# Optimization experiments

Hardware: AMD Instinct MI355X
Metric: run time of the kernel (lower is better)

## Reference

```python
import jax, jax.numpy as jnp
import numpy as np
import math

C = 256
GROUPS = 8
EPS = 1e-5


def setup_inputs() -> dict:
    key = jax.random.key(0)
    ks = jax.random.split(key, 12)
    b, c, h, w = 4, C, 64, 64
    s = 1.0 / math.sqrt(c)
    return {
        "x": jax.random.normal(ks[0], (b, c, h, w), dtype=jnp.float32),
        "gamma": jax.random.normal(ks[1], (c,), dtype=jnp.float32) * 0.1 + 1.0,
        "beta": jax.random.normal(ks[2], (c,), dtype=jnp.float32) * 0.1,
        "wq": jax.random.normal(ks[3], (c, c), dtype=jnp.float32) * s,
        "bq": jnp.zeros((c,), dtype=jnp.float32),
        "wk": jax.random.normal(ks[4], (c, c), dtype=jnp.float32) * s,
        "bk": jnp.zeros((c,), dtype=jnp.float32),
        "wv": jax.random.normal(ks[5], (c, c), dtype=jnp.float32) * s,
        "bv": jnp.zeros((c,), dtype=jnp.float32),
        "wp": jax.random.normal(ks[6], (c, c), dtype=jnp.float32) * s,
        "bp": jnp.zeros((c,), dtype=jnp.float32),
    }


def _group_norm(x, gamma, beta):
    b, c, h, w = x.shape
    xg = x.reshape(b, GROUPS, c // GROUPS, h * w)
    mean = xg.mean(axis=(2, 3), keepdims=True)
    var = xg.var(axis=(2, 3), keepdims=True)
    xn = ((xg - mean) * jax.lax.rsqrt(var + EPS)).reshape(b, c, h, w)
    return xn * gamma[None, :, None, None] + beta[None, :, None, None]


def _conv1x1(x, w, b):
    # 1x1 conv == per-pixel channel GEMM
    return jnp.einsum('oc,bchw->bohw', w, x) + b[None, :, None, None]


def reference(x, gamma, beta, wq, bq, wk, bk, wv, bv, wp, bp):
    b, c, h, w = x.shape
    n = h * w
    xn = _group_norm(x, gamma, beta)
    q = _conv1x1(xn, wq, bq).reshape(b, c, n)  # [b,c,n]
    k = _conv1x1(xn, wk, bk).reshape(b, c, n)
    v = _conv1x1(xn, wv, bv).reshape(b, c, n)
    scale = 1.0 / math.sqrt(c)
    scores = jnp.einsum('bcn,bcm->bnm', q, k) * scale  # [b,n,n]
    attn = jax.nn.softmax(scores, axis=-1)
    out = jnp.einsum('bnm,bcm->bcn', attn, v).reshape(b, c, h, w)
    return _conv1x1(out, wp, bp) + x
```

## Files before the change

kernel.cpp:

```cpp
#include <hip/hip_runtime.h>
#include <hip/hip_bf16.h>
#include <math.h>


#define CCH 256
#define NPIX 4096
#define NB 4
#define NG 8
#define EPS 1e-5f
#define NCHUNK 4

typedef __attribute__((ext_vector_type(8))) short short8;
typedef __attribute__((ext_vector_type(4))) short short4v;
typedef __attribute__((ext_vector_type(4))) float f32x4;
typedef __attribute__((ext_vector_type(16))) float f32x16;
typedef unsigned short ushort_t;
typedef unsigned char u8;

#define GLD16(g, l) __builtin_amdgcn_global_load_lds( \
    (const __attribute__((address_space(1))) unsigned int*)(g), \
    (__attribute__((address_space(3))) unsigned int*)(l), 16, 0, 0)

__device__ inline ushort_t f2bf(float x) {
    union { float f; unsigned u; } c; c.f = x;
    unsigned r = c.u + 0x7FFFu + ((c.u >> 16) & 1u);
    return (ushort_t)(r >> 16);
}
__device__ inline float bf2f(ushort_t h) {
    union { unsigned u; float f; } c; c.u = ((unsigned)h) << 16;
    return c.f;
}
__device__ inline u8 f2fp8(float x) {
    return (u8)(__builtin_amdgcn_cvt_pk_fp8_f32(x, x, 0, false) & 0xff);
}
__device__ inline long mk64(unsigned lo, unsigned hi) {
    return (long)(((unsigned long long)hi << 32) | lo);
}

__global__ __launch_bounds__(256) void gn1w(const float* __restrict__ x,
                                            const float* __restrict__ wq,
                                            const float* __restrict__ wk,
                                            const float* __restrict__ wv,
                                            const float* __restrict__ wp,
                                            float* __restrict__ part,
                                            ushort_t* __restrict__ wbf,
                                            ushort_t* __restrict__ wpbf) {
    int bid = blockIdx.x;
    int t = threadIdx.x;
    if (bid >= 256) {
        int widx = bid - 256;
        int wi = widx >> 6;
        const float* src = wi == 0 ? wq : wi == 1 ? wk : wi == 2 ? wv : wp;
        ushort_t* dst = wi == 3 ? wpbf : wbf + wi * 65536;
        int i = (widx & 63) * 1024 + t * 4;
        float4 v = *(const float4*)(src + i);
        short4v o;
        o[0] = (short)f2bf(v.x); o[1] = (short)f2bf(v.y);
        o[2] = (short)f2bf(v.z); o[3] = (short)f2bf(v.w);
        *(short4v*)(dst + i) = o;
        return;
    }
    int bg = bid >> 3;
    int slice = bid & 7;
    const float* base = x + (size_t)bg * 32 * NPIX + (size_t)slice * 16384;
    float s = 0.f, sq = 0.f;
    for (int i = t; i < 4096; i += 256) {
        float4 v = ((const float4*)base)[i];
        s  += v.x + v.y + v.z + v.w;
        sq += v.x*v.x + v.y*v.y + v.z*v.z + v.w*v.w;
    }
    for (int off = 32; off; off >>= 1) {
        s  += __shfl_down(s,  off);
        sq += __shfl_down(sq, off);
    }
    __shared__ float red[8];
    int wid = t >> 6;
    if ((t & 63) == 0) { red[wid*2] = s; red[wid*2+1] = sq; }
    __syncthreads();
    if (t == 0) {
        float ts = 0.f, tq = 0.f;
        for (int wv2 = 0; wv2 < 4; wv2++) { ts += red[wv2*2]; tq += red[wv2*2+1]; }
        part[bid*2] = ts; part[bid*2+1] = tq;
    }
}

__global__ __launch_bounds__(256) void gn_transpose(const float* __restrict__ x,
                                                    const float* __restrict__ part,
                                                    const float* __restrict__ gamma,
                                                    const float* __restrict__ beta,
                                                    ushort_t* __restrict__ xnT) {
    __shared__ float T[64][69];
    __shared__ float gmean[2], grstd[2];
    int t = threadIdx.x;
    int nBase = blockIdx.x * 64;
    int cBase = blockIdx.y * 64;
    int b = blockIdx.z;
    if (t < 2) {
        int g = (cBase >> 5) + t;
        float s = 0.f, sq = 0.f;
        for (int i = 0; i < 8; i++) {
            s  += part[((b*NG + g)*8 + i)*2];
            sq += part[((b*NG + g)*8 + i)*2 + 1];
        }
        const float inv = 1.f / 131072.f;
        float mean = s * inv;
        float var = sq * inv - mean * mean;
        gmean[t] = mean;
        grstd[t] = rsqrtf(var + EPS);
    }
    __syncthreads();
    const float* xb = x + (size_t)b * CCH * NPIX;
    int n4  = (t & 15) * 4;
    int cc0 = (t >> 4) * 4;
    for (int i = 0; i < 4; i++) {
        int cc = cc0 + i;
        int c = cBase + cc;
        int gi = cc >> 5;
        float ga = gamma[c] * grstd[gi];
        float be = beta[c] - gmean[gi] * ga;
        float4 v = *(const float4*)&xb[(size_t)c * NPIX + nBase + n4];
        T[cc][n4+0] = v.x * ga + be;
        T[cc][n4+1] = v.y * ga + be;
        T[cc][n4+2] = v.z * ga + be;
        T[cc][n4+3] = v.w * ga + be;
    }
    __syncthreads();
    int nn  = t >> 2;
    int ci0 = (t & 3) * 16;
    short8 o0, o1;
    for (int j = 0; j < 8; j++) {
        o0[j] = (short)f2bf(T[ci0 + j][nn]);
        o1[j] = (short)f2bf(T[ci0 + 8 + j][nn]);
    }
    ushort_t* dst = xnT + ((size_t)b * NPIX + nBase + nn) * CCH + cBase + ci0;
    *(short8*)dst = o0;
    *((short8*)dst + 1) = o1;
}

__global__ __launch_bounds__(256, 2) void qkv3(const ushort_t* __restrict__ xnT,
                                               const ushort_t* __restrict__ wbf,
                                               const float* __restrict__ bq,
                                               const float* __restrict__ bk,
                                               const float* __restrict__ bv,
                                               u8* __restrict__ qT,
                                               u8* __restrict__ kT,
                                               u8* __restrict__ vv) {
    __shared__ __align__(16) ushort_t As[2][4096];
    __shared__ __align__(16) ushort_t Bs[2][4096];
    int t = threadIdx.x;
    int w = t >> 6, l = t & 63, quad = l >> 4, l16 = l & 15;
    int z = blockIdx.z;
    const ushort_t* A; const ushort_t* B; int mBase, nBase;
    if (z < 2) { A = xnT; B = wbf + z * 65536; mBase = blockIdx.x * 128; nBase = blockIdx.y * 128; }
    else       { A = wbf + 131072; B = xnT;    mBase = blockIdx.y * 128; nBase = blockIdx.x * 128; }
    int m0 = (w & 1) * 64, n0 = (w >> 1) * 64;

    const f32x4 fz = {0.f, 0.f, 0.f, 0.f};
    f32x4 acc[4][4];
    #pragma unroll
    for (int i = 0; i < 4; i++)
        #pragma unroll
        for (int j = 0; j < 4; j++) acc[i][j] = fz;

    int srow = t >> 2;
    int slc  = (t & 3) ^ ((t >> 2) & 3);
    int sldso = (t >> 6) * 512;

    #pragma unroll
    for (int j = 0; j < 2; j++) {
        int row = 64*j + srow;
        GLD16(A + (size_t)(mBase + row) * 256 + slc * 8, &As[0][j*2048 + sldso]);
        GLD16(B + (size_t)(nBase + row) * 256 + slc * 8, &Bs[0][j*2048 + sldso]);
    }
    int buf = 0;
    for (int kb = 0; kb < 8; kb++) {
        __syncthreads();
        if (kb < 7) {
            #pragma unroll
            for (int j = 0; j < 2; j++) {
                int row = 64*j + srow;
                GLD16(A + (size_t)(mBase + row) * 256 + (kb+1)*32 + slc * 8, &As[buf^1][j*2048 + sldso]);
                GLD16(B + (size_t)(nBase + row) * 256 + (kb+1)*32 + slc * 8, &Bs[buf^1][j*2048 + sldso]);
            }
        }
        short8 af[4], bfr[4];
        #pragma unroll
        for (int mb = 0; mb < 4; mb++)
            af[mb] = *(short8*)&As[buf][(m0 + mb*16 + l16)*32 + ((quad ^ (l16 & 3)) * 8)];
        #pragma unroll
        for (int nb = 0; nb < 4; nb++)
            bfr[nb] = *(short8*)&Bs[buf][(n0 + nb*16 + l16)*32 + ((quad ^ (l16 & 3)) * 8)];
        #pragma unroll
        for (int mb = 0; mb < 4; mb++)
            #pragma unroll
            for (int nb = 0; nb < 4; nb++)
                acc[mb][nb] = __builtin_amdgcn_mfma_f32_16x16x32_bf16(af[mb], bfr[nb], acc[mb][nb], 0, 0, 0);
        buf ^= 1;
    }
    if (z < 2) {
        const float* bias = z ? bk : bq;
        u8* C = z ? kT : qT;
        #pragma unroll
        for (int nb = 0; nb < 4; nb++) {
            int n = nBase + n0 + nb*16 + l16;
            float bb = bias[n];
            #pragma unroll
            for (int mb = 0; mb < 4; mb++)
                #pragma unroll
                for (int r = 0; r < 4; r++) {
                    int m = mBase + m0 + mb*16 + quad*4 + r;
                    C[(size_t)m * 256 + n] = f2fp8(acc[mb][nb][r] + bb);
                }
        }
    } else {
        #pragma unroll
        for (int mb = 0; mb < 4; mb++)
            #pragma unroll
            for (int r = 0; r < 4; r++) {
                int m = mBase + m0 + mb*16 + quad*4 + r;
                float bb = bv[m];
                #pragma unroll
                for (int nb = 0; nb < 4; nb++) {
                    int n = nBase + n0 + nb*16 + l16;
                    vv[((size_t)(n >> 12) * 256 + m) * 4096 + (n & 4095)] = f2fp8(acc[mb][nb][r] + bb);
                }
            }
    }
}

__global__ __launch_bounds__(128, 2) void flash_attn(const u8* __restrict__ qT,
                                                     const u8* __restrict__ kT,
                                                     const u8* __restrict__ vv,
                                                     ushort_t* __restrict__ Op0,
                                                     ushort_t* __restrict__ Op1,
                                                     ushort_t* __restrict__ Op2,
                                                     ushort_t* __restrict__ Op3,
                                                     float* __restrict__ lsum) {
    __shared__ __align__(16) u8 Ks[2][8192];
    __shared__ __align__(16) u8 Vs[2][8192];
    int t = threadIdx.x;
    int w = t >> 6, l = t & 63;
    int l32 = l & 31, hl = l >> 5;
    int qBase = blockIdx.x * 64, chunk = blockIdx.y, b = blockIdx.z;
    int qw = qBase + w * 32;

    long qf[16];
    {
        const u8* qrow = qT + ((size_t)b * NPIX + qw + l32) * 256 + hl * 8;
        #pragma unroll
        for (int cb = 0; cb < 16; cb++) qf[cb] = *(const long*)(qrow + cb * 16);
    }

    f32x16 accO[8];
    #pragma unroll
    for (int i = 0; i < 8; i++)
        #pragma unroll
        for (int r = 0; r < 16; r++) accO[i][r] = 0.f;
    float lqa = 0.f;

    const u8* kbase = kT + (size_t)b * NPIX * 256;
    const u8* vbase = vv + (size_t)b * 256 * NPIX;

    const float SC = 0.0625f * 1.44269504089f;
    int mStart = chunk * (NPIX / NCHUNK);
    int mEnd = mStart + NPIX / NCHUNK;

    int kkv[4], kcb[4], vc[4], vs[4];
    #pragma unroll
    for (int j = 0; j < 4; j++) {
        int n = j*128 + t;
        kkv[j] = n >> 4; kcb[j] = (n & 15) ^ (kkv[j] & 15);
        vc[j]  = n >> 1; vs[j]  = (n & 1) ^ ((vc[j] >> 2) & 1);
    }

    #pragma unroll
    for (int j = 0; j < 4; j++) {
        int n = j*128 + t;
        GLD16(kbase + (size_t)(mStart + kkv[j]) * 256 + kcb[j] * 16, &Ks[0][n*16]);
        GLD16(vbase + (size_t)vc[j] * NPIX + mStart + vs[j] * 16, &Vs[0][n*16]);
    }
    int buf = 0;
    for (int mBase = mStart; mBase < mEnd; mBase += 32) {
        __syncthreads();
        if (mBase + 32 < mEnd) {
            #pragma unroll
            for (int j = 0; j < 4; j++) {
                int n = j*128 + t;
                GLD16(kbase + (size_t)(mBase + 32 + kkv[j]) * 256 + kcb[j] * 16, &Ks[buf^1][n*16]);
                GLD16(vbase + (size_t)vc[j] * NPIX + mBase + 32 + vs[j] * 16, &Vs[buf^1][n*16]);
            }
        }
        f32x16 sTa, sTb;
        #pragma unroll
        for (int r = 0; r < 16; r++) { sTa[r] = 0.f; sTb[r] = 0.f; }
        #pragma unroll
        for (int cb = 0; cb < 8; cb++) {
            long k0 = *(const long*)&Ks[buf][(l32*16 + (cb ^ (l32 & 15)))*16 + hl*8];
            long k1 = *(const long*)&Ks[buf][(l32*16 + ((cb+8) ^ (l32 & 15)))*16 + hl*8];
            sTa = __builtin_amdgcn_mfma_f32_32x32x16_fp8_fp8(k0, qf[cb],   sTa, 0, 0, 0);
            sTb = __builtin_amdgcn_mfma_f32_32x32x16_fp8_fp8(k1, qf[cb+8], sTb, 0, 0, 0);
        }
        float p[16];
        float part = 0.f;
        #pragma unroll
        for (int r = 0; r < 16; r++) {
            float pe = exp2f(fmaf(sTa[r] + sTb[r], SC, -5.0f));
            pe = fminf(pe, 240.f);
            p[r] = pe;
            part += pe;
        }
        lqa += part;
        unsigned pkd[4], swd[4];
        #pragma unroll
        for (int a = 0; a < 4; a++) {
            int u = __builtin_amdgcn_cvt_pk_fp8_f32(p[a*4+0], p[a*4+1], 0, false);
            u = __builtin_amdgcn_cvt_pk_fp8_f32(p[a*4+2], p[a*4+3], u, true);
            pkd[a] = (unsigned)u;
        }
        #pragma unroll
        for (int a = 0; a < 4; a++) swd[a] = (unsigned)__shfl_xor((int)pkd[a], 32);
        long B0 = hl == 0 ? mk64(pkd[0], swd[0]) : mk64(swd[1], pkd[1]);
        long B1 = hl == 0 ? mk64(pkd[2], swd[2]) : mk64(swd[3], pkd[3]);
        #pragma unroll
        for (int cblk = 0; cblk < 8; cblk++) {
            int c = cblk*32 + l32;
            int sw = (c >> 2) & 1;
            long v0 = *(const long*)&Vs[buf][(c*2 + sw)*16 + hl*8];
            long v1 = *(const long*)&Vs[buf][(c*2 + (1 ^ sw))*16 + hl*8];
            accO[cblk] = __builtin_amdgcn_mfma_f32_32x32x16_fp8_fp8(v0, B0, accO[cblk], 0, 0, 0);
            accO[cblk] = __builtin_amdgcn_mfma_f32_32x32x16_fp8_fp8(v1, B1, accO[cblk], 0, 0, 0);
        }
        buf ^= 1;
    }

    {
        float v = lqa + __shfl_xor(lqa, 32);
        if (hl == 0)
            lsum[((size_t)chunk * NB + b) * NPIX + qw + l32] = v;
    }
    ushort_t* op = chunk == 0 ? Op0 : chunk == 1 ? Op1 : chunk == 2 ? Op2 : Op3;
    size_t rowb = ((size_t)b * NPIX + qw + l32) * CCH;
    #pragma unroll
    for (int cblk = 0; cblk < 8; cblk++)
        #pragma unroll
        for (int a = 0; a < 4; a++) {
            short4v o;
            #pragma unroll
            for (int r = 0; r < 4; r++) o[r] = (short)f2bf(accO[cblk][a*4 + r]);
            *(short4v*)&op[rowb + cblk*32 + a*8 + hl*4] = o;
        }
}

__global__ __launch_bounds__(256) void attn_combine(ushort_t* __restrict__ Op0,
                                                    const ushort_t* __restrict__ Op1,
                                                    const ushort_t* __restrict__ Op2,
                                                    const ushort_t* __restrict__ Op3,
                                                    const float* __restrict__ lsum) {
    const size_t BN = (size_t)NB * NPIX;
    size_t base = ((size_t)blockIdx.x * 256 + threadIdx.x) * 4;
    size_t bn = base >> 8;
    float li = 1.f / (lsum[bn] + lsum[BN + bn] + lsum[2*BN + bn] + lsum[3*BN + bn]);
    short4v a0 = *(short4v*)&Op0[base];
    short4v a1 = *(const short4v*)&Op1[base];
    short4v a2 = *(const short4v*)&Op2[base];
    short4v a3 = *(const short4v*)&Op3[base];
    short4v o;
    #pragma unroll
    for (int i = 0; i < 4; i++) {
        float v = (bf2f((ushort_t)a0[i]) + bf2f((ushort_t)a1[i]) +
                   bf2f((ushort_t)a2[i]) + bf2f((ushort_t)a3[i])) * li;
        o[i] = (short)f2bf(v);
    }
    *(short4v*)&Op0[base] = o;
}

__global__ __launch_bounds__(256, 2) void projk(const ushort_t* __restrict__ wpbf,
                                                const ushort_t* __restrict__ aoT,
                                                const float* __restrict__ bp,
                                                const float* __restrict__ x,
                                                float* __restrict__ out) {
    __shared__ __align__(16) ushort_t As[2][4096];
    __shared__ __align__(16) ushort_t Bs[2][4096];
    int t = threadIdx.x;
    int w = t >> 6, l = t & 63, quad = l >> 4, l16 = l & 15;
    int mBase = blockIdx.y * 128, nBase = blockIdx.x * 128;
    int m0 = (w & 1) * 64, n0 = (w >> 1) * 64;

    const f32x4 fz = {0.f, 0.f, 0.f, 0.f};
    f32x4 acc[4][4];
    #pragma unroll
    for (int i = 0; i < 4; i++)
        #pragma unroll
        for (int j = 0; j < 4; j++) acc[i][j] = fz;

    int srow = t >> 2;
    int slc  = (t & 3) ^ ((t >> 2) & 3);
    int sldso = (t >> 6) * 512;

    #pragma unroll
    for (int j = 0; j < 2; j++) {
        int row = 64*j + srow;
        GLD16(wpbf + (size_t)(mBase + row) * 256 + slc * 8, &As[0][j*2048 + sldso]);
        GLD16(aoT  + (size_t)(nBase + row) * 256 + slc * 8, &Bs[0][j*2048 + sldso]);
    }
    int buf = 0;
    for (int kb = 0; kb < 8; kb++) {
        __syncthreads();
        if (kb < 7) {
            #pragma unroll
            for (int j = 0; j < 2; j++) {
                int row = 64*j + srow;
                GLD16(wpbf + (size_t)(mBase + row) * 256 + (kb+1)*32 + slc * 8, &As[buf^1][j*2048 + sldso]);
                GLD16(aoT  + (size_t)(nBase + row) * 256 + (kb+1)*32 + slc * 8, &Bs[buf^1][j*2048 + sldso]);
            }
        }
        short8 af[4], bfr[4];
        #pragma unroll
        for (int mb = 0; mb < 4; mb++)
            af[mb] = *(short8*)&As[buf][(m0 + mb*16 + l16)*32 + ((quad ^ (l16 & 3)) * 8)];
        #pragma unroll
        for (int nb = 0; nb < 4; nb++)
            bfr[nb] = *(short8*)&Bs[buf][(n0 + nb*16 + l16)*32 + ((quad ^ (l16 & 3)) * 8)];
        #pragma unroll
        for (int mb = 0; mb < 4; mb++)
            #pragma unroll
            for (int nb = 0; nb < 4; nb++)
                acc[mb][nb] = __builtin_amdgcn_mfma_f32_16x16x32_bf16(af[mb], bfr[nb], acc[mb][nb], 0, 0, 0);
        buf ^= 1;
    }
    #pragma unroll
    for (int mb = 0; mb < 4; mb++)
        #pragma unroll
        for (int r = 0; r < 4; r++) {
            int m = mBase + m0 + mb*16 + quad*4 + r;
            float bb = bp[m];
            #pragma unroll
            for (int nb = 0; nb < 4; nb++) {
                int n = nBase + n0 + nb*16 + l16;
                size_t idx = ((size_t)(n >> 12) * 256 + m) * 4096 + (n & 4095);
                out[idx] = acc[mb][nb][r] + bb + x[idx];
            }
        }
}

extern "C" void kernel_launch(void* const* d_in, const int* in_sizes, int n_in,
                              void* d_out, int out_size, void* d_ws, size_t ws_size,
                              hipStream_t stream) {
    const float* x     = (const float*)d_in[0];
    const float* gamma = (const float*)d_in[1];
    const float* beta  = (const float*)d_in[2];
    const float* wq    = (const float*)d_in[3];
    const float* bq    = (const float*)d_in[4];
    const float* wk    = (const float*)d_in[5];
    const float* bk    = (const float*)d_in[6];
    const float* wv    = (const float*)d_in[7];
    const float* bv    = (const float*)d_in[8];
    const float* wp    = (const float*)d_in[9];
    const float* bp    = (const float*)d_in[10];
    float* out = (float*)d_out;

    const size_t SZ = (size_t)NB * NPIX * CCH;
    float* part  = (float*)d_ws;
    float* lsum  = part + 512;
    ushort_t* wpbf = (ushort_t*)(lsum + (size_t)NCHUNK * NB * NPIX);
    ushort_t* slot0 = wpbf + 65536;
    ushort_t* Op3 = slot0;
    u8* qT8 = (u8*)(slot0 + SZ);
    u8* kT8 = (u8*)(slot0 + 2*SZ);
    u8* vv8 = (u8*)(slot0 + 3*SZ);
    ushort_t* aoT = slot0 + 4*SZ;
    ushort_t* xnT = (ushort_t*)d_out;
    ushort_t* Op1 = (ushort_t*)d_out;
    ushort_t* Op2 = (ushort_t*)d_out + SZ;
    ushort_t* wbf = (ushort_t*)d_out + SZ;

    gn1w<<<512, 256, 0, stream>>>(x, wq, wk, wv, wp, part, wbf, wpbf);
    gn_transpose<<<dim3(64, 4, 4), 256, 0, stream>>>(x, part, gamma, beta, xnT);
    qkv3<<<dim3(128, 2, 3), 256, 0, stream>>>(xnT, wbf, bq, bk, bv, qT8, kT8, vv8);
    flash_attn<<<dim3(64, NCHUNK, 4), 128, 0, stream>>>(qT8, kT8, vv8, aoT, Op1, Op2, Op3, lsum);
    attn_combine<<<(int)(SZ / 1024), 256, 0, stream>>>(aoT, Op1, Op2, Op3, lsum);
    projk<<<dim3(128, 2), 256, 0, stream>>>(wpbf, aoT, bp, x, out);
}
```

Baseline: 203.0 us.

## Software-pipeline QK^T of next tile with PV of current tile in flash attention

Restructures the attention loop so the QK^T MFMAs for tile t+1 are interleaved with the PV MFMAs for tile t, keeping the matrix units busy while the exp/convert/shuffle of the softmax runs. K stays double-buffered and V moves to a triple buffer with prefetch two tiles ahead. MFMA sections are wrapped in s_setprio. The change adds LDS use (one more 8KB V buffer), which may cut occupancy, and raises register pressure from holding both score and output accumulators live.

Result: no change. 201.8 us (-0.6%).

```diff
diff --git a/kernel.cpp b/kernel.cpp
--- a/kernel.cpp
+++ b/kernel.cpp
@@ -237,7 +237,7 @@
                                                      ushort_t* __restrict__ Op3,
                                                      float* __restrict__ lsum) {
     __shared__ __align__(16) u8 Ks[2][8192];
-    __shared__ __align__(16) u8 Vs[2][8192];
+    __shared__ __align__(16) u8 Vs[3][8192];
     int t = threadIdx.x;
     int w = t >> 6, l = t & 63;
     int l32 = l & 31, hl = l >> 5;
@@ -263,7 +263,7 @@
 
     const float SC = 0.0625f * 1.44269504089f;
     int mStart = chunk * (NPIX / NCHUNK);
-    int mEnd = mStart + NPIX / NCHUNK;
+    const int NT = (NPIX / NCHUNK) / 32;
 
     int kkv[4], kcb[4], vc[4], vs[4];
     #pragma unroll
@@ -278,38 +278,34 @@
         int n = j*128 + t;
         GLD16(kbase + (size_t)(mStart + kkv[j]) * 256 + kcb[j] * 16, &Ks[0][n*16]);
         GLD16(vbase + (size_t)vc[j] * NPIX + mStart + vs[j] * 16, &Vs[0][n*16]);
-    }
-    int buf = 0;
-    for (int mBase = mStart; mBase < mEnd; mBase += 32) {
-        __syncthreads();
-        if (mBase + 32 < mEnd) {
-            #pragma unroll
-            for (int j = 0; j < 4; j++) {
-                int n = j*128 + t;
-                GLD16(kbase + (size_t)(mBase + 32 + kkv[j]) * 256 + kcb[j] * 16, &Ks[buf^1][n*16]);
-                GLD16(vbase + (size_t)vc[j] * NPIX + mBase + 32 + vs[j] * 16, &Vs[buf^1][n*16]);
-            }
-        }
-        f32x16 sTa, sTb;
-        #pragma unroll
-        for (int r = 0; r < 16; r++) { sTa[r] = 0.f; sTb[r] = 0.f; }
-        #pragma unroll
-        for (int cb = 0; cb < 8; cb++) {
-            long k0 = *(const long*)&Ks[buf][(l32*16 + (cb ^ (l32 & 15)))*16 + hl*8];
-            long k1 = *(const long*)&Ks[buf][(l32*16 + ((cb+8) ^ (l32 & 15)))*16 + hl*8];
-            sTa = __builtin_amdgcn_mfma_f32_32x32x16_fp8_fp8(k0, qf[cb],   sTa, 0, 0, 0);
-            sTb = __builtin_amdgcn_mfma_f32_32x32x16_fp8_fp8(k1, qf[cb+8], sTb, 0, 0, 0);
-        }
+        GLD16(kbase + (size_t)(mStart + 32 + kkv[j]) * 256 + kcb[j] * 16, &Ks[1][n*16]);
+        GLD16(vbase + (size_t)vc[j] * NPIX + mStart + 32 + vs[j] * 16, &Vs[1][n*16]);
+    }
+    __syncthreads();
+
+    f32x16 sTa, sTb;
+    #pragma unroll
+    for (int r = 0; r < 16; r++) { sTa[r] = 0.f; sTb[r] = 0.f; }
+    #pragma unroll
+    for (int cb = 0; cb < 8; cb++) {
+        long k0 = *(const long*)&Ks[0][(l32*16 + (cb ^ (l32 & 15)))*16 + hl*8];
+        long k1 = *(const long*)&Ks[0][(l32*16 + ((cb+8) ^ (l32 & 15)))*16 + hl*8];
+        sTa = __builtin_amdgcn_mfma_f32_32x32x16_fp8_fp8(k0, qf[cb],   sTa, 0, 0, 0);
+        sTb = __builtin_amdgcn_mfma_f32_32x32x16_fp8_fp8(k1, qf[cb+8], sTb, 0, 0, 0);
+    }
+
+    int vcur = 0;
+    for (int tt = 0; tt < NT; tt++) {
         float p[16];
-        float part = 0.f;
+        float part0 = 0.f, part1 = 0.f;
         #pragma unroll
         for (int r = 0; r < 16; r++) {
             float pe = exp2f(fmaf(sTa[r] + sTb[r], SC, -5.0f));
             pe = fminf(pe, 240.f);
             p[r] = pe;
-            part += pe;
-        }
-        lqa += part;
+            if (r & 1) part1 += pe; else part0 += pe;
+        }
+        lqa += part0 + part1;
         unsigned pkd[4], swd[4];
         #pragma unroll
         for (int a = 0; a < 4; a++) {
@@ -321,16 +317,57 @@
         for (int a = 0; a < 4; a++) swd[a] = (unsigned)__shfl_xor((int)pkd[a], 32);
         long B0 = hl == 0 ? mk64(pkd[0], swd[0]) : mk64(swd[1], pkd[1]);
         long B1 = hl == 0 ? mk64(pkd[2], swd[2]) : mk64(swd[3], pkd[3]);
-        #pragma unroll
-        for (int cblk = 0; cblk < 8; cblk++) {
-            int c = cblk*32 + l32;
-            int sw = (c >> 2) & 1;
-            long v0 = *(const long*)&Vs[buf][(c*2 + sw)*16 + hl*8];
-            long v1 = *(const long*)&Vs[buf][(c*2 + (1 ^ sw))*16 + hl*8];
-            accO[cblk] = __builtin_amdgcn_mfma_f32_32x32x16_fp8_fp8(v0, B0, accO[cblk], 0, 0, 0);
-            accO[cblk] = __builtin_amdgcn_mfma_f32_32x32x16_fp8_fp8(v1, B1, accO[cblk], 0, 0, 0);
-        }
-        buf ^= 1;
+
+        __syncthreads();
+        if (tt + 2 < NT) {
+            int m2 = mStart + (tt + 2) * 32;
+            int vslot = vcur + 2; if (vslot >= 3) vslot -= 3;
+            #pragma unroll
+            for (int j = 0; j < 4; j++) {
+                int n = j*128 + t;
+                GLD16(kbase + (size_t)(m2 + kkv[j]) * 256 + kcb[j] * 16, &Ks[tt & 1][n*16]);
+                GLD16(vbase + (size_t)vc[j] * NPIX + m2 + vs[j] * 16, &Vs[vslot][n*16]);
+            }
+        }
+
+        __builtin_amdgcn_s_setprio(1);
+        if (tt < NT - 1) {
+            const u8* Kb = &Ks[(tt + 1) & 1][0];
+            const u8* Vb = &Vs[vcur][0];
+            #pragma unroll
+            for (int r = 0; r < 16; r++) { sTa[r] = 0.f; sTb[r] = 0.f; }
+            #pragma unroll
+            for (int cb = 0; cb < 8; cb++) {
+                long k0 = *(const long*)&Kb[(l32*16 + (cb ^ (l32 & 15)))*16 + hl*8];
+                int c = cb*32 + l32;
+                int sw = (c >> 2) & 1;
+                long v0 = *(const long*)&Vb[(c*2 + sw)*16 + hl*8];
+                sTa = __builtin_amdgcn_mfma_f32_32x32x16_fp8_fp8(k0, qf[cb], sTa, 0, 0, 0);
+                accO[cb] = __builtin_amdgcn_mfma_f32_32x32x16_fp8_fp8(v0, B0, accO[cb], 0, 0, 0);
+            }
+            #pragma unroll
+            for (int cb = 0; cb < 8; cb++) {
+                long k1 = *(const long*)&Kb[(l32*16 + ((cb+8) ^ (l32 & 15)))*16 + hl*8];
+                int c = cb*32 + l32;
+                int sw = (c >> 2) & 1;
+                long v1 = *(const long*)&Vb[(c*2 + (1 ^ sw))*16 + hl*8];
+                sTb = __builtin_amdgcn_mfma_f32_32x32x16_fp8_fp8(k1, qf[cb+8], sTb, 0, 0, 0);
+                accO[cb] = __builtin_amdgcn_mfma_f32_32x32x16_fp8_fp8(v1, B1, accO[cb], 0, 0, 0);
+            }
+        } else {
+            const u8* Vb = &Vs[vcur][0];
+            #pragma unroll
+            for (int cb = 0; cb < 8; cb++) {
+                int c = cb*32 + l32;
+                int sw = (c >> 2) & 1;
+                long v0 = *(const long*)&Vb[(c*2 + sw)*16 + hl*8];
+                long v1 = *(const long*)&Vb[(c*2 + (1 ^ sw))*16 + hl*8];
+                accO[cb] = __builtin_amdgcn_mfma_f32_32x32x16_fp8_fp8(v0, B0, accO[cb], 0, 0, 0);
+                accO[cb] = __builtin_amdgcn_mfma_f32_32x32x16_fp8_fp8(v1, B1, accO[cb], 0, 0, 0);
+            }
+        }
+        __builtin_amdgcn_s_setprio(0);
+        vcur = vcur + 1; if (vcur >= 3) vcur = 0;
     }
 
     {
```
